# Optimization experiments

Measured on AMD Instinct MI355X. Metric: run time of the kernel, lower is better.

Reference implementation:

```python
import jax, jax.numpy as jnp
import numpy as np

# ---- Build Cayley tables for projective GA G(3,0,1), basis ordered by grade ----
_BLADES = [(), (0,), (1,), (2,), (3,), (0,1), (0,2), (0,3), (1,2), (1,3), (2,3),
           (0,1,2), (0,1,3), (0,2,3), (1,2,3), (0,1,2,3)]
_IDX = {b: i for i, b in enumerate(_BLADES)}

def _blade_mul(a, b, metric):
    """Multiply basis blades a*b. Returns (sign, result_blade); sign=0 if it vanishes."""
    arr = list(a) + list(b)
    sign = 1
    changed = True
    while changed:
        changed = False
        for i in range(len(arr) - 1):
            if arr[i] > arr[i + 1]:
                arr[i], arr[i + 1] = arr[i + 1], arr[i]
                sign = -sign
                changed = True
            elif arr[i] == arr[i + 1]:
                sign *= metric[arr[i]]
                del arr[i:i + 2]
                changed = True
                break
    return sign, tuple(arr)

def _build_tables():
    metric = [0, 1, 1, 1]  # e0^2 = 0 (degenerate), e1^2=e2^2=e3^2=1
    G = np.zeros((16, 16, 16), np.float32)  # geometric product
    W = np.zeros((16, 16, 16), np.float32)  # outer (wedge) product
    for a in _BLADES:
        for b in _BLADES:
            s, r = _blade_mul(a, b, metric)
            if s != 0:
                G[_IDX[a], _IDX[b], _IDX[r]] = s
            if not (set(a) & set(b)):
                s2, r2 = _blade_mul(a, b, [1, 1, 1, 1])
                W[_IDX[a], _IDX[b], _IDX[r2]] = s2
    # Right-complement dual: dual(e_a) = s * e_c with e_a ^ dual(e_a) = e0123
    full = (0, 1, 2, 3)
    dual_idx = np.zeros(16, np.int32)
    dual_sign = np.zeros(16, np.float32)
    for a in _BLADES:
        c = tuple(sorted(set(full) - set(a)))
        s, _ = _blade_mul(a, c, [1, 1, 1, 1])
        dual_idx[_IDX[a]] = _IDX[c]
        dual_sign[_IDX[a]] = s
    # Coefficient map: dual(x)[j] = dual_sign[dual_idx[j]] * x[dual_idx[j]]
    out_sign = dual_sign[dual_idx]
    return jnp.asarray(G), jnp.asarray(W), jnp.asarray(dual_idx), jnp.asarray(out_sign)

_G, _W, _DUAL_IDX, _DUAL_SIGN = _build_tables()
_PSS = 15  # index of pseudoscalar e0123

def _dual(x):
    return x[..., _DUAL_IDX] * _DUAL_SIGN


def setup_inputs() -> dict:
    key = jax.random.key(0)
    k1, k2, k3 = jax.random.split(key, 3)
    B, T, C = 64, 8192, 16
    return {
        "x": jax.random.normal(k1, (B, T, C), dtype=jnp.float32),
        "y": jax.random.normal(k2, (B, T, C), dtype=jnp.float32),
        "ref": jax.random.normal(k3, (B, T, C), dtype=jnp.float32),
    }


def reference(x, y, ref):
    # Geometric product over the Cayley table
    gp = jnp.einsum("bti,btj,ijk->btk", x, y, _G)
    # E(3)-equivariant join: ref_e0123 * dual(dual(x) ^ dual(y))
    wedge = jnp.einsum("bti,btj,ijk->btk", _dual(x), _dual(y), _W)
    join = ref[..., _PSS:_PSS + 1] * _dual(wedge)
    return jnp.concatenate([gp, join], axis=-1)  # (B, T, 32)
```

## Files before the change

### kernel.cpp

```cpp
#include <hip/hip_runtime.h>

namespace ga {

constexpr int MASK[16]        = {0,1,2,4,8,3,5,9,6,10,12,7,11,13,14,15};
constexpr int IDX_OF_MASK[16] = {0,1,2,5,3,6,8,11,4,7,9,12,10,13,14,15};

constexpr int popc(int v) { int c = 0; while (v) { c += v & 1; v >>= 1; } return c; }

constexpr int reorder_sign(int a, int b) {
    int s = 0; int t = a >> 1;
    while (t) { s += popc(t & b); t >>= 1; }
    return (s & 1) ? -1 : 1;
}

struct Term { signed char i, j, k, s; };

struct GPTab { Term t[192]; };
constexpr GPTab build_gp() {
    GPTab T{}; int n = 0;
    for (int i = 0; i < 16; i++)
        for (int j = 0; j < 16; j++) {
            int a = MASK[i], b = MASK[j];
            if (a & b & 1) continue;
            T.t[n].i = (signed char)i;
            T.t[n].j = (signed char)j;
            T.t[n].k = (signed char)IDX_OF_MASK[a ^ b];
            T.t[n].s = (signed char)reorder_sign(a, b);
            n++;
        }
    return T;
}

struct JNTab { Term t[81]; };
constexpr JNTab build_join() {
    JNTab T{}; int n = 0;
    int didx[16] = {}, dsgn[16] = {};
    for (int i = 0; i < 16; i++) {
        int a = MASK[i], c = (~a) & 0xF;
        didx[i] = IDX_OF_MASK[c];
        dsgn[i] = reorder_sign(a, c);
    }
    for (int i = 0; i < 16; i++)
        for (int j = 0; j < 16; j++) {
            int p = didx[i], q = didx[j];
            int a = MASK[p], b = MASK[q];
            if (a & b) continue;
            int m = IDX_OF_MASK[a | b];
            int k = didx[m];
            int s = dsgn[i] * dsgn[j] * dsgn[m] * reorder_sign(a, b);
            T.t[n].i = (signed char)i;
            T.t[n].j = (signed char)j;
            T.t[n].k = (signed char)k;
            T.t[n].s = (signed char)s;
            n++;
        }
    return T;
}

constexpr GPTab G = build_gp();
constexpr JNTab J = build_join();

}

constexpr int BUF_FLOATS = 2304;
constexpr int OSTRIDE    = 36;

typedef const __attribute__((address_space(1))) void* gas_ptr;
typedef __attribute__((address_space(3))) void*       las_ptr;

__global__ __launch_bounds__(64, 4)
void MVGeometricBilinear_kernel(const float* __restrict__ x,
                                const float* __restrict__ y,
                                const float* __restrict__ ref,
                                float* __restrict__ out,
                                int nchunks)
{
    __shared__ __align__(16) float buf[BUF_FLOATS];
    __shared__ __align__(16) float rbuf[64];

    const int lane = threadIdx.x;
    const long chunk = blockIdx.x;
    if (chunk >= nchunks) return;

    {
        const float4* gx = reinterpret_cast<const float4*>(x) + chunk * 256;
        const float4* gy = reinterpret_cast<const float4*>(y) + chunk * 256;
#pragma unroll
        for (int k = 0; k < 4; k++) {
            __builtin_amdgcn_global_load_lds((gas_ptr)(gx + k * 64 + lane),
                                             (las_ptr)(&buf[k * 256]), 16, 0, 0);
            __builtin_amdgcn_global_load_lds((gas_ptr)(gy + k * 64 + lane),
                                             (las_ptr)(&buf[1024 + k * 256]), 16, 0, 0);
        }
        __builtin_amdgcn_global_load_lds((gas_ptr)(ref + (chunk * 64 + lane) * 16 + 15),
                                         (las_ptr)(&rbuf[0]), 4, 0, 0);
    }

    asm volatile("s_waitcnt vmcnt(0)" ::: "memory");

    const float* bx = &buf[0];
    const float* by = &buf[1024];
    float xx[16], yy[16];
#pragma unroll
    for (int k = 0; k < 4; k++) {
        const float4 vx = *reinterpret_cast<const float4*>(bx + lane * 16 + k * 4);
        const float4 vy = *reinterpret_cast<const float4*>(by + lane * 16 + k * 4);
        xx[4*k+0] = vx.x; xx[4*k+1] = vx.y; xx[4*k+2] = vx.z; xx[4*k+3] = vx.w;
        yy[4*k+0] = vy.x; yy[4*k+1] = vy.y; yy[4*k+2] = vy.z; yy[4*k+3] = vy.w;
    }
    const float r = rbuf[lane];

    float gp[16] = {0.f, 0.f, 0.f, 0.f, 0.f, 0.f, 0.f, 0.f,
                    0.f, 0.f, 0.f, 0.f, 0.f, 0.f, 0.f, 0.f};
    float jn[16] = {0.f, 0.f, 0.f, 0.f, 0.f, 0.f, 0.f, 0.f,
                    0.f, 0.f, 0.f, 0.f, 0.f, 0.f, 0.f, 0.f};
#pragma unroll
    for (int t = 0; t < 192; t++) {
        const int ti = ga::G.t[t].i, tj = ga::G.t[t].j, tk = ga::G.t[t].k;
        const float v = xx[ti] * yy[tj];
        if (ga::G.t[t].s > 0) gp[tk] += v; else gp[tk] -= v;
    }
#pragma unroll
    for (int t = 0; t < 81; t++) {
        const int ti = ga::J.t[t].i, tj = ga::J.t[t].j, tk = ga::J.t[t].k;
        const float v = xx[ti] * yy[tj];
        if (ga::J.t[t].s > 0) jn[tk] += v; else jn[tk] -= v;
    }

    asm volatile("" ::: "memory");

    float* lo = &buf[0];
#pragma unroll
    for (int k = 0; k < 4; k++)
        *reinterpret_cast<float4*>(lo + lane * OSTRIDE + k * 4) =
            make_float4(gp[4*k+0], gp[4*k+1], gp[4*k+2], gp[4*k+3]);
#pragma unroll
    for (int k = 0; k < 4; k++)
        *reinterpret_cast<float4*>(lo + lane * OSTRIDE + 16 + k * 4) =
            make_float4(r * jn[4*k+0], r * jn[4*k+1], r * jn[4*k+2], r * jn[4*k+3]);

    float4* go = reinterpret_cast<float4*>(out) + chunk * 512;
#pragma unroll
    for (int c = 0; c < 8; c++) {
        const int g  = lane + 64 * c;
        const int p  = g >> 3;
        const int ch = g & 7;
        go[g] = *reinterpret_cast<const float4*>(lo + p * OSTRIDE + ch * 4);
    }
}

__global__ __launch_bounds__(64)
void MVGeometricBilinear_tail(const float* __restrict__ x,
                              const float* __restrict__ y,
                              const float* __restrict__ ref,
                              float* __restrict__ out,
                              int start, int npts)
{
    int pt = start + blockIdx.x * 64 + threadIdx.x;
    if (pt >= npts) return;
    float xx[16], yy[16];
#pragma unroll
    for (int k = 0; k < 16; k++) { xx[k] = x[(size_t)pt*16+k]; yy[k] = y[(size_t)pt*16+k]; }
    const float r = ref[(size_t)pt*16+15];
    float gp[16] = {}, jn[16] = {};
#pragma unroll
    for (int t = 0; t < 192; t++) {
        const float v = xx[ga::G.t[t].i] * yy[ga::G.t[t].j];
        if (ga::G.t[t].s > 0) gp[ga::G.t[t].k] += v; else gp[ga::G.t[t].k] -= v;
    }
#pragma unroll
    for (int t = 0; t < 81; t++) {
        const float v = xx[ga::J.t[t].i] * yy[ga::J.t[t].j];
        if (ga::J.t[t].s > 0) jn[ga::J.t[t].k] += v; else jn[ga::J.t[t].k] -= v;
    }
#pragma unroll
    for (int k = 0; k < 16; k++) out[(size_t)pt*32+k] = gp[k];
#pragma unroll
    for (int k = 0; k < 16; k++) out[(size_t)pt*32+16+k] = r * jn[k];
}

extern "C" void kernel_launch(void* const* d_in, const int* in_sizes, int n_in,
                              void* d_out, int out_size, void* d_ws, size_t ws_size,
                              hipStream_t stream) {
    const float* x   = (const float*)d_in[0];
    const float* y   = (const float*)d_in[1];
    const float* ref = (const float*)d_in[2];
    float* out = (float*)d_out;

    const int npts    = in_sizes[0] / 16;
    const int nchunks = npts / 64;

    if (nchunks > 0) {
        MVGeometricBilinear_kernel<<<nchunks, 64, 0, stream>>>(
            x, y, ref, out, nchunks);
    }

    const int rem = npts - nchunks * 64;
    if (rem > 0) {
        MVGeometricBilinear_tail<<<(rem + 63) / 64, 64, 0, stream>>>(
            x, y, ref, out, nchunks * 64, npts);
    }
}
```

Before: 144.8 us.

## Replace LDS-staged chunk kernel with direct per-thread global loads and stores

Removes the shared-memory staging path: each thread now loads its own point's x/y as float4 directly from global memory and writes its 32 outputs as float4 directly, instead of using global_load_lds plus an LDS transpose for coalesced stores. Block size goes from 64 to 256 with a single launch and a bounds check, so the separate tail kernel is dropped. The GP and join are computed in separate scopes so each can be stored before the other is built, which lowers register pressure. The trade-off is that loads and stores are strided per lane (64 B and 128 B per thread), relying on the caches to merge them rather than on explicit coalescing.

```diff
diff --git a/kernel.cpp b/kernel.cpp
--- a/kernel.cpp
+++ b/kernel.cpp
@@ -62,121 +62,59 @@
 
 }
 
-constexpr int BUF_FLOATS = 2304;
-constexpr int OSTRIDE    = 36;
 
-typedef const __attribute__((address_space(1))) void* gas_ptr;
-typedef __attribute__((address_space(3))) void*       las_ptr;
-
-__global__ __launch_bounds__(64, 4)
+__global__ __launch_bounds__(256, 6)
 void MVGeometricBilinear_kernel(const float* __restrict__ x,
                                 const float* __restrict__ y,
                                 const float* __restrict__ ref,
                                 float* __restrict__ out,
-                                int nchunks)
+                                int npts)
 {
-    __shared__ __align__(16) float buf[BUF_FLOATS];
-    __shared__ __align__(16) float rbuf[64];
+    const int pt = blockIdx.x * 256 + threadIdx.x;
+    if (pt >= npts) return;
 
-    const int lane = threadIdx.x;
-    const long chunk = blockIdx.x;
-    if (chunk >= nchunks) return;
-
-    {
-        const float4* gx = reinterpret_cast<const float4*>(x) + chunk * 256;
-        const float4* gy = reinterpret_cast<const float4*>(y) + chunk * 256;
-#pragma unroll
-        for (int k = 0; k < 4; k++) {
-            __builtin_amdgcn_global_load_lds((gas_ptr)(gx + k * 64 + lane),
-                                             (las_ptr)(&buf[k * 256]), 16, 0, 0);
-            __builtin_amdgcn_global_load_lds((gas_ptr)(gy + k * 64 + lane),
-                                             (las_ptr)(&buf[1024 + k * 256]), 16, 0, 0);
-        }
-        __builtin_amdgcn_global_load_lds((gas_ptr)(ref + (chunk * 64 + lane) * 16 + 15),
-                                         (las_ptr)(&rbuf[0]), 4, 0, 0);
-    }
-
-    asm volatile("s_waitcnt vmcnt(0)" ::: "memory");
-
-    const float* bx = &buf[0];
-    const float* by = &buf[1024];
+    const float4* xp = reinterpret_cast<const float4*>(x) + (size_t)pt * 4;
+    const float4* yp = reinterpret_cast<const float4*>(y) + (size_t)pt * 4;
     float xx[16], yy[16];
 #pragma unroll
     for (int k = 0; k < 4; k++) {
-        const float4 vx = *reinterpret_cast<const float4*>(bx + lane * 16 + k * 4);
-        const float4 vy = *reinterpret_cast<const float4*>(by + lane * 16 + k * 4);
+        const float4 vx = xp[k];
+        const float4 vy = yp[k];
         xx[4*k+0] = vx.x; xx[4*k+1] = vx.y; xx[4*k+2] = vx.z; xx[4*k+3] = vx.w;
         yy[4*k+0] = vy.x; yy[4*k+1] = vy.y; yy[4*k+2] = vy.z; yy[4*k+3] = vy.w;
     }
-    const float r = rbuf[lane];
+    const float r = ref[(size_t)pt * 16 + 15];
 
-    float gp[16] = {0.f, 0.f, 0.f, 0.f, 0.f, 0.f, 0.f, 0.f,
-                    0.f, 0.f, 0.f, 0.f, 0.f, 0.f, 0.f, 0.f};
-    float jn[16] = {0.f, 0.f, 0.f, 0.f, 0.f, 0.f, 0.f, 0.f,
-                    0.f, 0.f, 0.f, 0.f, 0.f, 0.f, 0.f, 0.f};
+    float4* op = reinterpret_cast<float4*>(out) + (size_t)pt * 8;
+
+    {
+        float gp[16] = {0.f, 0.f, 0.f, 0.f, 0.f, 0.f, 0.f, 0.f,
+                        0.f, 0.f, 0.f, 0.f, 0.f, 0.f, 0.f, 0.f};
 #pragma unroll
-    for (int t = 0; t < 192; t++) {
-        const int ti = ga::G.t[t].i, tj = ga::G.t[t].j, tk = ga::G.t[t].k;
-        const float v = xx[ti] * yy[tj];
-        if (ga::G.t[t].s > 0) gp[tk] += v; else gp[tk] -= v;
-    }
+        for (int t = 0; t < 192; t++) {
+            const int ti = ga::G.t[t].i, tj = ga::G.t[t].j, tk = ga::G.t[t].k;
+            const float v = xx[ti] * yy[tj];
+            if (ga::G.t[t].s > 0) gp[tk] += v; else gp[tk] -= v;
+        }
 #pragma unroll
-    for (int t = 0; t < 81; t++) {
-        const int ti = ga::J.t[t].i, tj = ga::J.t[t].j, tk = ga::J.t[t].k;
-        const float v = xx[ti] * yy[tj];
-        if (ga::J.t[t].s > 0) jn[tk] += v; else jn[tk] -= v;
+        for (int k = 0; k < 4; k++)
+            op[k] = make_float4(gp[4*k+0], gp[4*k+1], gp[4*k+2], gp[4*k+3]);
     }
 
-    asm volatile("" ::: "memory");
-
-    float* lo = &buf[0];
+    {
+        float jn[16] = {0.f, 0.f, 0.f, 0.f, 0.f, 0.f, 0.f, 0.f,
+                        0.f, 0.f, 0.f, 0.f, 0.f, 0.f, 0.f, 0.f};
 #pragma unroll
-    for (int k = 0; k < 4; k++)
-        *reinterpret_cast<float4*>(lo + lane * OSTRIDE + k * 4) =
-            make_float4(gp[4*k+0], gp[4*k+1], gp[4*k+2], gp[4*k+3]);
+        for (int t = 0; t < 81; t++) {
+            const int ti = ga::J.t[t].i, tj = ga::J.t[t].j, tk = ga::J.t[t].k;
+            const float v = xx[ti] * yy[tj];
+            if (ga::J.t[t].s > 0) jn[tk] += v; else jn[tk] -= v;
+        }
 #pragma unroll
-    for (int k = 0; k < 4; k++)
-        *reinterpret_cast<float4*>(lo + lane * OSTRIDE + 16 + k * 4) =
-            make_float4(r * jn[4*k+0], r * jn[4*k+1], r * jn[4*k+2], r * jn[4*k+3]);
-
-    float4* go = reinterpret_cast<float4*>(out) + chunk * 512;
-#pragma unroll
-    for (int c = 0; c < 8; c++) {
-        const int g  = lane + 64 * c;
-        const int p  = g >> 3;
-        const int ch = g & 7;
-        go[g] = *reinterpret_cast<const float4*>(lo + p * OSTRIDE + ch * 4);
+        for (int k = 0; k < 4; k++)
+            op[4 + k] = make_float4(r * jn[4*k+0], r * jn[4*k+1],
+                                    r * jn[4*k+2], r * jn[4*k+3]);
     }
-}
-
-__global__ __launch_bounds__(64)
-void MVGeometricBilinear_tail(const float* __restrict__ x,
-                              const float* __restrict__ y,
-                              const float* __restrict__ ref,
-                              float* __restrict__ out,
-                              int start, int npts)
-{
-    int pt = start + blockIdx.x * 64 + threadIdx.x;
-    if (pt >= npts) return;
-    float xx[16], yy[16];
-#pragma unroll
-    for (int k = 0; k < 16; k++) { xx[k] = x[(size_t)pt*16+k]; yy[k] = y[(size_t)pt*16+k]; }
-    const float r = ref[(size_t)pt*16+15];
-    float gp[16] = {}, jn[16] = {};
-#pragma unroll
-    for (int t = 0; t < 192; t++) {
-        const float v = xx[ga::G.t[t].i] * yy[ga::G.t[t].j];
-        if (ga::G.t[t].s > 0) gp[ga::G.t[t].k] += v; else gp[ga::G.t[t].k] -= v;
-    }
-#pragma unroll
-    for (int t = 0; t < 81; t++) {
-        const float v = xx[ga::J.t[t].i] * yy[ga::J.t[t].j];
-        if (ga::J.t[t].s > 0) jn[ga::J.t[t].k] += v; else jn[ga::J.t[t].k] -= v;
-    }
-#pragma unroll
-    for (int k = 0; k < 16; k++) out[(size_t)pt*32+k] = gp[k];
-#pragma unroll
-    for (int k = 0; k < 16; k++) out[(size_t)pt*32+16+k] = r * jn[k];
 }
 
 extern "C" void kernel_launch(void* const* d_in, const int* in_sizes, int n_in,
@@ -187,17 +125,11 @@
     const float* ref = (const float*)d_in[2];
     float* out = (float*)d_out;
 
-    const int npts    = in_sizes[0] / 16;
-    const int nchunks = npts / 64;
+    const int npts   = in_sizes[0] / 16;
+    const int blocks = (npts + 255) / 256;
 
-    if (nchunks > 0) {
-        MVGeometricBilinear_kernel<<<nchunks, 64, 0, stream>>>(
-            x, y, ref, out, nchunks);
-    }
-
-    const int rem = npts - nchunks * 64;
-    if (rem > 0) {
-        MVGeometricBilinear_tail<<<(rem + 63) / 64, 64, 0, stream>>>(
-            x, y, ref, out, nchunks * 64, npts);
+    if (npts > 0) {
+        MVGeometricBilinear_kernel<<<blocks, 256, 0, stream>>>(
+            x, y, ref, out, npts);
     }
 }
```

After: 206.1 us. +42.4%, slower.

## Double-buffer LDS DMA across multiple chunks per block and split work across two waves

Applied to the files above, without the earlier changes.

The kernel now launches a capped grid of 128-thread blocks, and each block walks up to four chunks with a grid stride. The global_load_lds copy of the next chunk is issued into a second LDS buffer while the current chunk is computed and stored. Each wave loads one operand (x or y) and computes half of the output components. LDS access is swizzled on load and on the output staging to avoid bank conflicts. The aim is to hide memory latency and raise the bandwidth in flight, at the cost of extra barriers, manual vmcnt bookkeeping and fewer resident blocks.

```diff
diff --git a/kernel.cpp b/kernel.cpp
--- a/kernel.cpp
+++ b/kernel.cpp
@@ -62,90 +62,150 @@
 
 }
 
-constexpr int BUF_FLOATS = 2304;
-constexpr int OSTRIDE    = 36;
 
 typedef const __attribute__((address_space(1))) void* gas_ptr;
 typedef __attribute__((address_space(3))) void*       las_ptr;
 
-__global__ __launch_bounds__(64, 4)
+constexpr int NITER = 4;
+
+template<int HALF>
+__device__ __forceinline__ void accum_half(const float* __restrict__ xx,
+                                           const float* __restrict__ yy,
+                                           float* __restrict__ acc,
+                                           float* __restrict__ jacc)
+{
+#pragma unroll
+    for (int t = 0; t < 192; t++) {
+        const int tk = ga::G.t[t].k;
+        if ((tk < 8) != (HALF == 0)) continue;
+        const float v = xx[ga::G.t[t].i] * yy[ga::G.t[t].j];
+        if (ga::G.t[t].s > 0) acc[tk & 7] += v; else acc[tk & 7] -= v;
+    }
+#pragma unroll
+    for (int t = 0; t < 81; t++) {
+        const int tk = ga::J.t[t].k;
+        if ((tk < 8) != (HALF == 0)) continue;
+        const float v = xx[ga::J.t[t].i] * yy[ga::J.t[t].j];
+        if (ga::J.t[t].s > 0) jacc[tk & 7] += v; else jacc[tk & 7] -= v;
+    }
+}
+
+__global__ __launch_bounds__(128, 4)
 void MVGeometricBilinear_kernel(const float* __restrict__ x,
                                 const float* __restrict__ y,
                                 const float* __restrict__ ref,
                                 float* __restrict__ out,
-                                int nchunks)
+                                int nchunks, int gstride)
 {
-    __shared__ __align__(16) float buf[BUF_FLOATS];
-    __shared__ __align__(16) float rbuf[64];
-
-    const int lane = threadIdx.x;
-    const long chunk = blockIdx.x;
-    if (chunk >= nchunks) return;
-
+    __shared__ __align__(16) float buf[2][2048];
+
+    const int tid  = threadIdx.x;
+    const int lane = tid & 63;
+    const int wid  = tid >> 6;
+
+    const long chunk0 = blockIdx.x;
+    if (chunk0 >= nchunks) return;
+
+    float rr[NITER];
     {
-        const float4* gx = reinterpret_cast<const float4*>(x) + chunk * 256;
-        const float4* gy = reinterpret_cast<const float4*>(y) + chunk * 256;
-#pragma unroll
-        for (int k = 0; k < 4; k++) {
-            __builtin_amdgcn_global_load_lds((gas_ptr)(gx + k * 64 + lane),
-                                             (las_ptr)(&buf[k * 256]), 16, 0, 0);
-            __builtin_amdgcn_global_load_lds((gas_ptr)(gy + k * 64 + lane),
-                                             (las_ptr)(&buf[1024 + k * 256]), 16, 0, 0);
-        }
-        __builtin_amdgcn_global_load_lds((gas_ptr)(ref + (chunk * 64 + lane) * 16 + 15),
-                                         (las_ptr)(&rbuf[0]), 4, 0, 0);
-    }
-
-    asm volatile("s_waitcnt vmcnt(0)" ::: "memory");
-
-    const float* bx = &buf[0];
-    const float* by = &buf[1024];
-    float xx[16], yy[16];
-#pragma unroll
-    for (int k = 0; k < 4; k++) {
-        const float4 vx = *reinterpret_cast<const float4*>(bx + lane * 16 + k * 4);
-        const float4 vy = *reinterpret_cast<const float4*>(by + lane * 16 + k * 4);
-        xx[4*k+0] = vx.x; xx[4*k+1] = vx.y; xx[4*k+2] = vx.z; xx[4*k+3] = vx.w;
-        yy[4*k+0] = vy.x; yy[4*k+1] = vy.y; yy[4*k+2] = vy.z; yy[4*k+3] = vy.w;
-    }
-    const float r = rbuf[lane];
-
-    float gp[16] = {0.f, 0.f, 0.f, 0.f, 0.f, 0.f, 0.f, 0.f,
-                    0.f, 0.f, 0.f, 0.f, 0.f, 0.f, 0.f, 0.f};
-    float jn[16] = {0.f, 0.f, 0.f, 0.f, 0.f, 0.f, 0.f, 0.f,
-                    0.f, 0.f, 0.f, 0.f, 0.f, 0.f, 0.f, 0.f};
-#pragma unroll
-    for (int t = 0; t < 192; t++) {
-        const int ti = ga::G.t[t].i, tj = ga::G.t[t].j, tk = ga::G.t[t].k;
-        const float v = xx[ti] * yy[tj];
-        if (ga::G.t[t].s > 0) gp[tk] += v; else gp[tk] -= v;
-    }
-#pragma unroll
-    for (int t = 0; t < 81; t++) {
-        const int ti = ga::J.t[t].i, tj = ga::J.t[t].j, tk = ga::J.t[t].k;
-        const float v = xx[ti] * yy[tj];
-        if (ga::J.t[t].s > 0) jn[tk] += v; else jn[tk] -= v;
-    }
-
-    asm volatile("" ::: "memory");
-
-    float* lo = &buf[0];
-#pragma unroll
-    for (int k = 0; k < 4; k++)
-        *reinterpret_cast<float4*>(lo + lane * OSTRIDE + k * 4) =
-            make_float4(gp[4*k+0], gp[4*k+1], gp[4*k+2], gp[4*k+3]);
-#pragma unroll
-    for (int k = 0; k < 4; k++)
-        *reinterpret_cast<float4*>(lo + lane * OSTRIDE + 16 + k * 4) =
-            make_float4(r * jn[4*k+0], r * jn[4*k+1], r * jn[4*k+2], r * jn[4*k+3]);
-
-    float4* go = reinterpret_cast<float4*>(out) + chunk * 512;
-#pragma unroll
-    for (int c = 0; c < 8; c++) {
-        const int g  = lane + 64 * c;
-        const int p  = g >> 3;
-        const int ch = g & 7;
-        go[g] = *reinterpret_cast<const float4*>(lo + p * OSTRIDE + ch * 4);
+        long c = chunk0;
+#pragma unroll
+        for (int it = 0; it < NITER; ++it) {
+            if (c < nchunks) rr[it] = ref[(c * 64 + lane) * 16 + 15];
+            c += gstride;
+        }
+    }
+
+    int srcoff[4];
+    int fragoff[4];
+#pragma unroll
+    for (int k = 0; k < 4; ++k) {
+        const int slot = k * 64 + lane;
+        const int j = ((slot & 3) - ((slot >> 3) & 3)) & 3;
+        srcoff[k] = (slot & ~3) | j;
+        const int s = (k + ((lane >> 1) & 3)) & 3;
+        fragoff[k] = lane * 16 + (s << 2);
+    }
+
+    const float4* gsrc = reinterpret_cast<const float4*>(wid ? y : x);
+    const int ldsbase = wid ? 1024 : 0;
+
+    auto dma = [&](long c, int b) {
+#pragma unroll
+        for (int k = 0; k < 4; ++k)
+            __builtin_amdgcn_global_load_lds(
+                (gas_ptr)(gsrc + c * 256 + srcoff[k]),
+                (las_ptr)(&buf[b][ldsbase + k * 256]), 16, 0, 0);
+    };
+
+    long chunk = chunk0;
+    int cur = 0;
+    dma(chunk, 0);
+
+#pragma unroll
+    for (int it = 0; it < NITER; ++it) {
+        const long next = chunk + gstride;
+        const bool pf = (it + 1 < NITER) && (next < nchunks);
+        if (pf) dma(next, cur ^ 1);
+
+        if (it == 0) {
+            if (pf) asm volatile("s_waitcnt vmcnt(4)" ::: "memory");
+            else    asm volatile("s_waitcnt vmcnt(0)" ::: "memory");
+        } else {
+            if (pf) asm volatile("s_waitcnt vmcnt(8)" ::: "memory");
+            else    asm volatile("s_waitcnt vmcnt(4)" ::: "memory");
+        }
+        __builtin_amdgcn_s_barrier();
+
+        float xx[16], yy[16];
+#pragma unroll
+        for (int k = 0; k < 4; ++k) {
+            const float4 vx = *reinterpret_cast<const float4*>(&buf[cur][fragoff[k]]);
+            const float4 vy = *reinterpret_cast<const float4*>(&buf[cur][1024 + fragoff[k]]);
+            xx[4*k+0] = vx.x; xx[4*k+1] = vx.y; xx[4*k+2] = vx.z; xx[4*k+3] = vx.w;
+            yy[4*k+0] = vy.x; yy[4*k+1] = vy.y; yy[4*k+2] = vy.z; yy[4*k+3] = vy.w;
+        }
+        asm volatile("s_waitcnt lgkmcnt(0)" ::: "memory");
+        __builtin_amdgcn_s_barrier();
+
+        float acc[8]  = {0.f,0.f,0.f,0.f,0.f,0.f,0.f,0.f};
+        float jacc[8] = {0.f,0.f,0.f,0.f,0.f,0.f,0.f,0.f};
+        if (wid == 0) accum_half<0>(xx, yy, acc, jacc);
+        else          accum_half<1>(xx, yy, acc, jacc);
+        const float r = rr[it];
+
+        {
+            float* lo = &buf[cur][0];
+            const int pb = lane * 32, px = lane & 7;
+            const int qg = 2 * wid, qj = 4 + 2 * wid;
+            *reinterpret_cast<float4*>(lo + pb + (((qg    ) ^ px) << 2)) =
+                make_float4(acc[0], acc[1], acc[2], acc[3]);
+            *reinterpret_cast<float4*>(lo + pb + (((qg + 1) ^ px) << 2)) =
+                make_float4(acc[4], acc[5], acc[6], acc[7]);
+            *reinterpret_cast<float4*>(lo + pb + (((qj    ) ^ px) << 2)) =
+                make_float4(r*jacc[0], r*jacc[1], r*jacc[2], r*jacc[3]);
+            *reinterpret_cast<float4*>(lo + pb + (((qj + 1) ^ px) << 2)) =
+                make_float4(r*jacc[4], r*jacc[5], r*jacc[6], r*jacc[7]);
+        }
+        asm volatile("s_waitcnt lgkmcnt(0)" ::: "memory");
+        __builtin_amdgcn_s_barrier();
+
+        {
+            float4* go = reinterpret_cast<float4*>(out) + chunk * 512;
+#pragma unroll
+            for (int c = 0; c < 4; ++c) {
+                const int g = c * 128 + wid * 64 + lane;
+                const int p = g >> 3, q = g & 7;
+                go[g] = *reinterpret_cast<const float4*>(
+                            &buf[cur][p * 32 + ((q ^ (p & 7)) << 2)]);
+            }
+        }
+        asm volatile("s_waitcnt lgkmcnt(0)" ::: "memory");
+        __builtin_amdgcn_s_barrier();
+
+        if (!pf) break;
+        cur ^= 1;
+        chunk = next;
     }
 }
 
@@ -191,8 +251,11 @@
     const int nchunks = npts / 64;
 
     if (nchunks > 0) {
-        MVGeometricBilinear_kernel<<<nchunks, 64, 0, stream>>>(
-            x, y, ref, out, nchunks);
+        int blocks = nchunks < 2560 ? nchunks : 2560;
+        const int need = (nchunks + NITER - 1) / NITER;
+        if (blocks < need) blocks = need;
+        MVGeometricBilinear_kernel<<<blocks, 128, 0, stream>>>(
+            x, y, ref, out, nchunks, blocks);
     }
 
     const int rem = npts - nchunks * 64;
```

Measured after the change: 147.6 us. Within noise of the previous version (+2.0%).

## Load inputs directly to registers, pack four waves per block, swizzle output staging

Applied to the files above, without the earlier changes.

Drops the global_load_lds staging of x/y/ref and has each lane read its own multivector straight into registers with float4 loads. Blocks now hold four independent 64-lane waves, with a per-wave LDS region. The output transpose uses an XOR-swizzled 32-float stride instead of padding, and the final global writes are nontemporal. The goal is to cut LDS traffic and launch overhead and to stop output writes from polluting the cache. The trade-off is per-lane strided global reads (64 bytes per lane) in place of fully coalesced wave-wide loads.

```diff
diff --git a/kernel.cpp b/kernel.cpp
--- a/kernel.cpp
+++ b/kernel.cpp
@@ -62,90 +62,79 @@
 
 }
 
-constexpr int BUF_FLOATS = 2304;
-constexpr int OSTRIDE    = 36;
 
-typedef const __attribute__((address_space(1))) void* gas_ptr;
-typedef __attribute__((address_space(3))) void*       las_ptr;
+typedef float f32x4 __attribute__((ext_vector_type(4)));
 
-__global__ __launch_bounds__(64, 4)
+__global__ __launch_bounds__(256, 5)
 void MVGeometricBilinear_kernel(const float* __restrict__ x,
                                 const float* __restrict__ y,
                                 const float* __restrict__ ref,
                                 float* __restrict__ out,
                                 int nchunks)
 {
-    __shared__ __align__(16) float buf[BUF_FLOATS];
-    __shared__ __align__(16) float rbuf[64];
+    __shared__ __align__(16) float lds[4][2048];
 
-    const int lane = threadIdx.x;
-    const long chunk = blockIdx.x;
+    const int lane = threadIdx.x & 63;
+    const int wid  = threadIdx.x >> 6;
+    const long chunk = (long)blockIdx.x * 4 + wid;
     if (chunk >= nchunks) return;
+    const long pt = chunk * 64 + lane;
 
-    {
-        const float4* gx = reinterpret_cast<const float4*>(x) + chunk * 256;
-        const float4* gy = reinterpret_cast<const float4*>(y) + chunk * 256;
-#pragma unroll
-        for (int k = 0; k < 4; k++) {
-            __builtin_amdgcn_global_load_lds((gas_ptr)(gx + k * 64 + lane),
-                                             (las_ptr)(&buf[k * 256]), 16, 0, 0);
-            __builtin_amdgcn_global_load_lds((gas_ptr)(gy + k * 64 + lane),
-                                             (las_ptr)(&buf[1024 + k * 256]), 16, 0, 0);
-        }
-        __builtin_amdgcn_global_load_lds((gas_ptr)(ref + (chunk * 64 + lane) * 16 + 15),
-                                         (las_ptr)(&rbuf[0]), 4, 0, 0);
-    }
-
-    asm volatile("s_waitcnt vmcnt(0)" ::: "memory");
-
-    const float* bx = &buf[0];
-    const float* by = &buf[1024];
+    const float4* xp = reinterpret_cast<const float4*>(x) + pt * 4;
+    const float4* yp = reinterpret_cast<const float4*>(y) + pt * 4;
     float xx[16], yy[16];
 #pragma unroll
     for (int k = 0; k < 4; k++) {
-        const float4 vx = *reinterpret_cast<const float4*>(bx + lane * 16 + k * 4);
-        const float4 vy = *reinterpret_cast<const float4*>(by + lane * 16 + k * 4);
+        const float4 vx = xp[k];
+        const float4 vy = yp[k];
         xx[4*k+0] = vx.x; xx[4*k+1] = vx.y; xx[4*k+2] = vx.z; xx[4*k+3] = vx.w;
         yy[4*k+0] = vy.x; yy[4*k+1] = vy.y; yy[4*k+2] = vy.z; yy[4*k+3] = vy.w;
     }
-    const float r = rbuf[lane];
+    const float r = ref[pt * 16 + 15];
 
-    float gp[16] = {0.f, 0.f, 0.f, 0.f, 0.f, 0.f, 0.f, 0.f,
-                    0.f, 0.f, 0.f, 0.f, 0.f, 0.f, 0.f, 0.f};
-    float jn[16] = {0.f, 0.f, 0.f, 0.f, 0.f, 0.f, 0.f, 0.f,
-                    0.f, 0.f, 0.f, 0.f, 0.f, 0.f, 0.f, 0.f};
+    float* lo = &lds[wid][0];
+    const int px = lane & 7;
+
+    {
+        float gp[16] = {0.f,0.f,0.f,0.f,0.f,0.f,0.f,0.f,
+                        0.f,0.f,0.f,0.f,0.f,0.f,0.f,0.f};
 #pragma unroll
-    for (int t = 0; t < 192; t++) {
-        const int ti = ga::G.t[t].i, tj = ga::G.t[t].j, tk = ga::G.t[t].k;
-        const float v = xx[ti] * yy[tj];
-        if (ga::G.t[t].s > 0) gp[tk] += v; else gp[tk] -= v;
-    }
+        for (int t = 0; t < 192; t++) {
+            const int ti = ga::G.t[t].i, tj = ga::G.t[t].j, tk = ga::G.t[t].k;
+            const float v = xx[ti] * yy[tj];
+            if (ga::G.t[t].s > 0) gp[tk] += v; else gp[tk] -= v;
+        }
 #pragma unroll
-    for (int t = 0; t < 81; t++) {
-        const int ti = ga::J.t[t].i, tj = ga::J.t[t].j, tk = ga::J.t[t].k;
-        const float v = xx[ti] * yy[tj];
-        if (ga::J.t[t].s > 0) jn[tk] += v; else jn[tk] -= v;
+        for (int q = 0; q < 4; q++)
+            *reinterpret_cast<float4*>(lo + lane * 32 + ((q ^ px) << 2)) =
+                make_float4(gp[4*q+0], gp[4*q+1], gp[4*q+2], gp[4*q+3]);
     }
 
-    asm volatile("" ::: "memory");
+    {
+        float jn[16] = {0.f,0.f,0.f,0.f,0.f,0.f,0.f,0.f,
+                        0.f,0.f,0.f,0.f,0.f,0.f,0.f,0.f};
+#pragma unroll
+        for (int t = 0; t < 81; t++) {
+            const int ti = ga::J.t[t].i, tj = ga::J.t[t].j, tk = ga::J.t[t].k;
+            const float v = xx[ti] * yy[tj];
+            if (ga::J.t[t].s > 0) jn[tk] += v; else jn[tk] -= v;
+        }
+#pragma unroll
+        for (int q = 0; q < 4; q++)
+            *reinterpret_cast<float4*>(lo + lane * 32 + (((q + 4) ^ px) << 2)) =
+                make_float4(r*jn[4*q+0], r*jn[4*q+1], r*jn[4*q+2], r*jn[4*q+3]);
+    }
 
-    float* lo = &buf[0];
-#pragma unroll
-    for (int k = 0; k < 4; k++)
-        *reinterpret_cast<float4*>(lo + lane * OSTRIDE + k * 4) =
-            make_float4(gp[4*k+0], gp[4*k+1], gp[4*k+2], gp[4*k+3]);
-#pragma unroll
-    for (int k = 0; k < 4; k++)
-        *reinterpret_cast<float4*>(lo + lane * OSTRIDE + 16 + k * 4) =
-            make_float4(r * jn[4*k+0], r * jn[4*k+1], r * jn[4*k+2], r * jn[4*k+3]);
+    asm volatile("s_waitcnt lgkmcnt(0)" ::: "memory");
 
-    float4* go = reinterpret_cast<float4*>(out) + chunk * 512;
+    f32x4* go = reinterpret_cast<f32x4*>(out) + chunk * 512;
 #pragma unroll
     for (int c = 0; c < 8; c++) {
-        const int g  = lane + 64 * c;
-        const int p  = g >> 3;
-        const int ch = g & 7;
-        go[g] = *reinterpret_cast<const float4*>(lo + p * OSTRIDE + ch * 4);
+        const int g = c * 64 + lane;
+        const int p = g >> 3, q = g & 7;
+        const f32x4 v = *reinterpret_cast<const f32x4*>(
+                            lo + p * 32 + ((q ^ (p & 7)) << 2));
+        __builtin_nontemporal_store(v, go + g);
     }
 }
 
@@ -191,7 +180,8 @@
     const int nchunks = npts / 64;
 
     if (nchunks > 0) {
-        MVGeometricBilinear_kernel<<<nchunks, 64, 0, stream>>>(
+        const int blocks = (nchunks + 3) / 4;
+        MVGeometricBilinear_kernel<<<blocks, 256, 0, stream>>>(
             x, y, ref, out, nchunks);
     }
 
```

Result: slower. 153.6 us (+6.1%).
